# Optimization experiments

Measured on AMD Instinct MI355X. Metric: run time of the kernel, lower is better.

## Reference

```python
import jax, jax.numpy as jnp
import numpy as np

HIDDEN = 1024
EMB = 256
VOCAB = 500000
B = 4096
C = 128
EPS = 1e-12


def setup_inputs() -> dict:
    key = jax.random.key(0)
    ks = jax.random.split(key, 8)
    hidden_states = jax.random.normal(ks[0], (B, HIDDEN), dtype=jnp.float32)
    cand_idx = jax.random.randint(ks[1], (B, C), 0, VOCAB, dtype=jnp.int32)
    W_dense = jax.random.normal(ks[2], (EMB, HIDDEN), dtype=jnp.float32) * (1.0 / np.sqrt(HIDDEN))
    b_dense = jnp.zeros((EMB,), dtype=jnp.float32)
    ln_gamma = jnp.ones((EMB,), dtype=jnp.float32)
    ln_beta = jnp.zeros((EMB,), dtype=jnp.float32)
    decoder_table = jax.random.normal(ks[3], (VOCAB, EMB), dtype=jnp.float32) * 0.02
    entity_bias = jnp.zeros((VOCAB,), dtype=jnp.float32)
    return {
        "hidden_states": hidden_states,
        "W_dense": W_dense,
        "b_dense": b_dense,
        "ln_gamma": ln_gamma,
        "ln_beta": ln_beta,
        "decoder_table": decoder_table,
        "entity_bias": entity_bias,
        "cand_idx": cand_idx,
    }


def _transform(x, W_dense, b_dense, ln_gamma, ln_beta):
    # Linear hidden_size -> entity_emb_size, gelu, LayerNorm
    h = x @ W_dense.T + b_dense
    h = jax.nn.gelu(h, approximate=False)
    mu = jnp.mean(h, axis=-1, keepdims=True)
    var = jnp.mean(jnp.square(h - mu), axis=-1, keepdims=True)
    return (h - mu) * jax.lax.rsqrt(var + EPS) * ln_gamma + ln_beta


def reference(hidden_states, W_dense, b_dense, ln_gamma, ln_beta, decoder_table, entity_bias, cand_idx):
    h = _transform(hidden_states, W_dense, b_dense, ln_gamma, ln_beta)  # [B, EMB]
    cand_emb = decoder_table[cand_idx]          # [B, C, EMB] ragged gather (padded)
    bias = entity_bias[cand_idx]                # [B, C]
    scores = jnp.einsum('bce,be->bc', cand_emb, h) + bias  # [B, C]
    return scores
```

## Files before the change

kernel.cpp:

```cpp
#include <hip/hip_runtime.h>
#include <hip/hip_bf16.h>
#include <math.h>

#define HIDDEN 1024
#define EMB    256
#define BROWS  4096
#define CAND   128
#define LN_EPS 1e-12f

typedef __attribute__((ext_vector_type(8))) short bf16x8;
typedef __attribute__((ext_vector_type(4))) float f32x4;

__device__ __forceinline__ int swz(int row, int slot) { return slot ^ ((row >> 1) & 3); }

__device__ __forceinline__ unsigned short f2bf(float f) {
    __bf16 h = (__bf16)f;
    return __builtin_bit_cast(unsigned short, h);
}

__global__ __launch_bounds__(256) void k_transform(
    const float* __restrict__ A,
    const float* __restrict__ W,
    const float* __restrict__ bias,
    const float* __restrict__ gamma,
    const float* __restrict__ beta,
    float* __restrict__ G)
{
    __shared__ unsigned short As[16 * 32];
    __shared__ unsigned short Ws[256 * 32];
    __shared__ float part[16][8];

    const int tid  = threadIdx.x;
    const int lane = tid & 63;
    const int wv   = tid >> 6;
    const int m0   = blockIdx.x * 16;

    const int lcol = lane & 15;
    const int lk   = lane >> 4;

    f32x4 acc[4] = {};

    for (int kt = 0; kt < HIDDEN; kt += 32) {
        float4 a0, a1;
        const int arow = tid >> 2, apr = tid & 3;
        if (tid < 64) {
            a0 = *(const float4*)&A[(size_t)(m0 + arow) * HIDDEN + kt + apr * 8];
            a1 = *(const float4*)&A[(size_t)(m0 + arow) * HIDDEN + kt + apr * 8 + 4];
        }
        float4 w0[4], w1[4];
        #pragma unroll
        for (int i = 0; i < 4; ++i) {
            int id = tid + i * 256;
            int row = id >> 2, pr = id & 3;
            w0[i] = *(const float4*)&W[(size_t)row * HIDDEN + kt + pr * 8];
            w1[i] = *(const float4*)&W[(size_t)row * HIDDEN + kt + pr * 8 + 4];
        }
        __syncthreads();
        if (tid < 64) {
            bf16x8 v;
            v[0]=f2bf(a0.x); v[1]=f2bf(a0.y); v[2]=f2bf(a0.z); v[3]=f2bf(a0.w);
            v[4]=f2bf(a1.x); v[5]=f2bf(a1.y); v[6]=f2bf(a1.z); v[7]=f2bf(a1.w);
            *(bf16x8*)&As[arow * 32 + swz(arow, apr) * 8] = v;
        }
        #pragma unroll
        for (int i = 0; i < 4; ++i) {
            int id = tid + i * 256;
            int row = id >> 2, pr = id & 3;
            bf16x8 v;
            v[0]=f2bf(w0[i].x); v[1]=f2bf(w0[i].y); v[2]=f2bf(w0[i].z); v[3]=f2bf(w0[i].w);
            v[4]=f2bf(w1[i].x); v[5]=f2bf(w1[i].y); v[6]=f2bf(w1[i].z); v[7]=f2bf(w1[i].w);
            *(bf16x8*)&Ws[row * 32 + swz(row, pr) * 8] = v;
        }
        __syncthreads();
        bf16x8 af = *(const bf16x8*)&As[lcol * 32 + swz(lcol, lk) * 8];
        bf16x8 bfr[4];
        #pragma unroll
        for (int n = 0; n < 4; ++n) {
            int r = wv * 64 + n * 16 + lcol;
            bfr[n] = *(const bf16x8*)&Ws[r * 32 + swz(r, lk) * 8];
        }
        #pragma unroll
        for (int n = 0; n < 4; ++n)
            acc[n] = __builtin_amdgcn_mfma_f32_16x16x32_bf16(af, bfr[n], acc[n], 0, 0, 0);
    }

    float bcol[4], gcol[4], becol[4];
    #pragma unroll
    for (int n = 0; n < 4; ++n) {
        int col = wv * 64 + n * 16 + lcol;
        bcol[n]  = bias[col];
        gcol[n]  = gamma[col];
        becol[n] = beta[col];
    }

    float sv[4] = {}, qv[4] = {};
    #pragma unroll
    for (int n = 0; n < 4; ++n) {
        #pragma unroll
        for (int r = 0; r < 4; ++r) {
            float v = acc[n][r] + bcol[n];
            v = 0.5f * v * (1.0f + erff(v * 0.70710678118654752f));
            acc[n][r] = v;
            sv[r] += v;
            qv[r] += v * v;
        }
    }
    #pragma unroll
    for (int r = 0; r < 4; ++r) {
        #pragma unroll
        for (int msk = 8; msk >= 1; msk >>= 1) {
            sv[r] += __shfl_xor(sv[r], msk);
            qv[r] += __shfl_xor(qv[r], msk);
        }
    }
    if (lcol == 0) {
        #pragma unroll
        for (int r = 0; r < 4; ++r) {
            int R = lk * 4 + r;
            part[R][wv * 2 + 0] = sv[r];
            part[R][wv * 2 + 1] = qv[r];
        }
    }
    __syncthreads();

    #pragma unroll
    for (int r = 0; r < 4; ++r) {
        int R = lk * 4 + r;
        float4 p0 = *(const float4*)&part[R][0];
        float4 p1 = *(const float4*)&part[R][4];
        float s  = p0.x + p0.z + p1.x + p1.z;
        float q  = p0.y + p0.w + p1.y + p1.w;
        float mu = s * (1.0f / 256.0f);
        float var = q * (1.0f / 256.0f) - mu * mu;
        float rs = rsqrtf(var + LN_EPS);
        #pragma unroll
        for (int n = 0; n < 4; ++n) {
            int col = wv * 64 + n * 16 + lcol;
            G[(size_t)(m0 + R) * EMB + col] = (acc[n][r] - mu) * rs * gcol[n] + becol[n];
        }
    }
}

__global__ __launch_bounds__(256) void k_scores(
    const float* __restrict__ H,
    const float* __restrict__ table,
    const float* __restrict__ ebias,
    const int*   __restrict__ cidx,
    float* __restrict__ out)
{
    const int b    = blockIdx.x;
    const int tid  = threadIdx.x;
    const int lane = tid & 63;
    const int wv   = tid >> 6;
    const int l    = lane & 15;
    const int q    = lane >> 4;

    const float4* Hrow = (const float4*)(H + (size_t)b * EMB);
    float4 hv[4];
    #pragma unroll
    for (int p = 0; p < 4; ++p) hv[p] = Hrow[p * 16 + l];

    const int cbase = wv * 32 + q;
    int idxs[8];
    #pragma unroll
    for (int it = 0; it < 8; ++it)
        idxs[it] = cidx[(size_t)b * CAND + cbase + it * 4];

    #pragma unroll
    for (int it = 0; it < 8; ++it) {
        const float4* row = (const float4*)(table + (size_t)idxs[it] * EMB);
        float4 t0 = row[ 0 + l];
        float4 t1 = row[16 + l];
        float4 t2 = row[32 + l];
        float4 t3 = row[48 + l];
        float  eb = ebias[idxs[it]];
        float s = t0.x*hv[0].x + t0.y*hv[0].y + t0.z*hv[0].z + t0.w*hv[0].w
                + t1.x*hv[1].x + t1.y*hv[1].y + t1.z*hv[1].z + t1.w*hv[1].w
                + t2.x*hv[2].x + t2.y*hv[2].y + t2.z*hv[2].z + t2.w*hv[2].w
                + t3.x*hv[3].x + t3.y*hv[3].y + t3.z*hv[3].z + t3.w*hv[3].w;
        #pragma unroll
        for (int m = 8; m >= 1; m >>= 1) s += __shfl_xor(s, m);
        if (l == 0) out[(size_t)b * CAND + cbase + it * 4] = s + eb;
    }
}

extern "C" void kernel_launch(void* const* d_in, const int* in_sizes, int n_in,
                              void* d_out, int out_size, void* d_ws, size_t ws_size,
                              hipStream_t stream) {
    const float* hidden = (const float*)d_in[0];
    const float* Wd     = (const float*)d_in[1];
    const float* bd     = (const float*)d_in[2];
    const float* gamma  = (const float*)d_in[3];
    const float* beta   = (const float*)d_in[4];
    const float* table  = (const float*)d_in[5];
    const float* ebias  = (const float*)d_in[6];
    const int*   cidx   = (const int*)d_in[7];
    float* out = (float*)d_out;

    float* G = (float*)d_ws;

    k_transform<<<dim3(BROWS / 16), 256, 0, stream>>>(hidden, Wd, bd, gamma, beta, G);
    k_scores<<<dim3(BROWS), 256, 0, stream>>>(G, table, ebias, cidx, out);
}
```

Measured before the change: 135.6 us.

## Bucket-sort candidate entries by vocab index to improve table gather locality

Adds a counting-sort pipeline (zero, per-block histogram, single-block scan, scatter) that groups all B*C candidate entries into 1024 buckets by vocab index range. The gather kernel then processes entries in bucket order, so nearby table rows are fetched together and should hit in cache more often, with a block index swizzle spread across XCDs. The transformed hidden state is stored in bf16 to shrink the per-entry H reads that now become random. The cost is four extra launches, atomics, scattered output writes, and reduced precision of h.

```diff
diff --git a/kernel.cpp b/kernel.cpp
--- a/kernel.cpp
+++ b/kernel.cpp
@@ -8,6 +8,11 @@
 #define CAND   128
 #define LN_EPS 1e-12f
 
+#define NENT   (BROWS * CAND)
+#define NB     1024
+#define BKT_SH 9
+
+typedef unsigned int u32;
 typedef __attribute__((ext_vector_type(8))) short bf16x8;
 typedef __attribute__((ext_vector_type(4))) float f32x4;
 
@@ -16,6 +21,9 @@
 __device__ __forceinline__ unsigned short f2bf(float f) {
     __bf16 h = (__bf16)f;
     return __builtin_bit_cast(unsigned short, h);
+}
+__device__ __forceinline__ float bf2f(unsigned short u) {
+    return __builtin_bit_cast(float, (u32)u << 16);
 }
 
 __global__ __launch_bounds__(256) void k_transform(
@@ -24,7 +32,7 @@
     const float* __restrict__ bias,
     const float* __restrict__ gamma,
     const float* __restrict__ beta,
-    float* __restrict__ G)
+    unsigned short* __restrict__ Hbf)
 {
     __shared__ unsigned short As[16 * 32];
     __shared__ unsigned short Ws[256 * 32];
@@ -136,51 +144,130 @@
         #pragma unroll
         for (int n = 0; n < 4; ++n) {
             int col = wv * 64 + n * 16 + lcol;
-            G[(size_t)(m0 + R) * EMB + col] = (acc[n][r] - mu) * rs * gcol[n] + becol[n];
-        }
-    }
-}
-
-__global__ __launch_bounds__(256) void k_scores(
-    const float* __restrict__ H,
+            Hbf[(size_t)(m0 + R) * EMB + col] = f2bf((acc[n][r] - mu) * rs * gcol[n] + becol[n]);
+        }
+    }
+}
+
+__global__ __launch_bounds__(256) void k_zero(u32* __restrict__ bkt_pad)
+{
+    bkt_pad[blockIdx.x * 256 + threadIdx.x] = 0;
+}
+
+__global__ __launch_bounds__(256) void k_count(
+    const int* __restrict__ cidx, u32* __restrict__ bkt_pad)
+{
+    __shared__ u32 lh[NB];
+    const int tid = threadIdx.x;
+    for (int t = tid; t < NB; t += 256) lh[t] = 0;
+    __syncthreads();
+    const int base = blockIdx.x * 8192;
+    #pragma unroll
+    for (int i = 0; i < 32; ++i) {
+        int idx = cidx[base + i * 256 + tid];
+        atomicAdd(&lh[idx >> BKT_SH], 1u);
+    }
+    __syncthreads();
+    for (int t = tid; t < NB; t += 256) {
+        u32 v = lh[t];
+        if (v) atomicAdd(&bkt_pad[t * 16], v);
+    }
+}
+
+__global__ __launch_bounds__(1024) void k_scan(u32* __restrict__ bkt_pad)
+{
+    __shared__ u32 a[NB];
+    const int t = threadIdx.x;
+    const u32 own = bkt_pad[t * 16];
+    a[t] = own;
+    __syncthreads();
+    for (int off = 1; off < NB; off <<= 1) {
+        u32 add = (t >= off) ? a[t - off] : 0u;
+        __syncthreads();
+        a[t] += add;
+        __syncthreads();
+    }
+    bkt_pad[t * 16] = a[t] - own;
+}
+
+__global__ __launch_bounds__(256) void k_scatter(
+    const int* __restrict__ cidx, u32* __restrict__ bkt_pad,
+    u32* __restrict__ ent_idx, u32* __restrict__ ent_e)
+{
+    __shared__ u32 lh[NB];
+    __shared__ u32 lb[NB];
+    __shared__ u32 lo[NB];
+    const int tid = threadIdx.x;
+    for (int t = tid; t < NB; t += 256) { lh[t] = 0; lo[t] = 0; }
+    __syncthreads();
+    const int base = blockIdx.x * 8192;
+    u32 iv[32];
+    #pragma unroll
+    for (int i = 0; i < 32; ++i) {
+        iv[i] = (u32)cidx[base + i * 256 + tid];
+        atomicAdd(&lh[iv[i] >> BKT_SH], 1u);
+    }
+    __syncthreads();
+    for (int t = tid; t < NB; t += 256) {
+        u32 v = lh[t];
+        if (v) lb[t] = atomicAdd(&bkt_pad[t * 16], v);
+    }
+    __syncthreads();
+    #pragma unroll
+    for (int i = 0; i < 32; ++i) {
+        u32 bkt = iv[i] >> BKT_SH;
+        u32 p = lb[bkt] + atomicAdd(&lo[bkt], 1u);
+        ent_idx[p] = iv[i];
+        ent_e[p]   = (u32)(base + i * 256 + tid);
+    }
+}
+
+__global__ __launch_bounds__(256) void k_gather(
+    const unsigned short* __restrict__ Hbf,
     const float* __restrict__ table,
     const float* __restrict__ ebias,
-    const int*   __restrict__ cidx,
+    const u32* __restrict__ ent_idx,
+    const u32* __restrict__ ent_e,
     float* __restrict__ out)
 {
-    const int b    = blockIdx.x;
+    const int bid  = blockIdx.x;
+    const int work = (bid & 7) * 512 + (bid >> 3);
     const int tid  = threadIdx.x;
     const int lane = tid & 63;
     const int wv   = tid >> 6;
     const int l    = lane & 15;
     const int q    = lane >> 4;
 
-    const float4* Hrow = (const float4*)(H + (size_t)b * EMB);
-    float4 hv[4];
-    #pragma unroll
-    for (int p = 0; p < 4; ++p) hv[p] = Hrow[p * 16 + l];
-
-    const int cbase = wv * 32 + q;
-    int idxs[8];
-    #pragma unroll
-    for (int it = 0; it < 8; ++it)
-        idxs[it] = cidx[(size_t)b * CAND + cbase + it * 4];
+    const int ebase = work * 128 + wv * 32 + q;
+    u32 idxs[8], es[8];
+    #pragma unroll
+    for (int it = 0; it < 8; ++it) {
+        idxs[it] = ent_idx[ebase + it * 4];
+        es[it]   = ent_e[ebase + it * 4];
+    }
 
     #pragma unroll
     for (int it = 0; it < 8; ++it) {
         const float4* row = (const float4*)(table + (size_t)idxs[it] * EMB);
+        const u32 e = es[it];
+        const unsigned short* hrow = Hbf + (size_t)(e >> 7) * EMB;
+
         float4 t0 = row[ 0 + l];
         float4 t1 = row[16 + l];
         float4 t2 = row[32 + l];
         float4 t3 = row[48 + l];
-        float  eb = ebias[idxs[it]];
-        float s = t0.x*hv[0].x + t0.y*hv[0].y + t0.z*hv[0].z + t0.w*hv[0].w
-                + t1.x*hv[1].x + t1.y*hv[1].y + t1.z*hv[1].z + t1.w*hv[1].w
-                + t2.x*hv[2].x + t2.y*hv[2].y + t2.z*hv[2].z + t2.w*hv[2].w
-                + t3.x*hv[3].x + t3.y*hv[3].y + t3.z*hv[3].z + t3.w*hv[3].w;
+        ushort4 h0 = *(const ushort4*)&hrow[  0 + l * 4];
+        ushort4 h1 = *(const ushort4*)&hrow[ 64 + l * 4];
+        ushort4 h2 = *(const ushort4*)&hrow[128 + l * 4];
+        ushort4 h3 = *(const ushort4*)&hrow[192 + l * 4];
+
+        float s = t0.x*bf2f(h0.x) + t0.y*bf2f(h0.y) + t0.z*bf2f(h0.z) + t0.w*bf2f(h0.w)
+                + t1.x*bf2f(h1.x) + t1.y*bf2f(h1.y) + t1.z*bf2f(h1.z) + t1.w*bf2f(h1.w)
+                + t2.x*bf2f(h2.x) + t2.y*bf2f(h2.y) + t2.z*bf2f(h2.z) + t2.w*bf2f(h2.w)
+                + t3.x*bf2f(h3.x) + t3.y*bf2f(h3.y) + t3.z*bf2f(h3.z) + t3.w*bf2f(h3.w);
         #pragma unroll
         for (int m = 8; m >= 1; m >>= 1) s += __shfl_xor(s, m);
-        if (l == 0) out[(size_t)b * CAND + cbase + it * 4] = s + eb;
+        if (l == 0) out[e] = s + ebias[idxs[it]];
     }
 }
 
@@ -197,8 +284,16 @@
     const int*   cidx   = (const int*)d_in[7];
     float* out = (float*)d_out;
 
-    float* G = (float*)d_ws;
-
-    k_transform<<<dim3(BROWS / 16), 256, 0, stream>>>(hidden, Wd, bd, gamma, beta, G);
-    k_scores<<<dim3(BROWS), 256, 0, stream>>>(G, table, ebias, cidx, out);
-}
+    char* ws = (char*)d_ws;
+    unsigned short* Hbf  = (unsigned short*)(ws);
+    u32* bkt_pad         = (u32*)(ws + 2097152);
+    u32* ent_idx         = (u32*)(ws + 2097152 + 65536);
+    u32* ent_e           = (u32*)(ws + 2097152 + 65536 + 2097152);
+
+    k_transform<<<dim3(BROWS / 16), 256, 0, stream>>>(hidden, Wd, bd, gamma, beta, Hbf);
+    k_zero<<<dim3(64), 256, 0, stream>>>(bkt_pad);
+    k_count<<<dim3(64), 256, 0, stream>>>(cidx, bkt_pad);
+    k_scan<<<dim3(1), 1024, 0, stream>>>(bkt_pad);
+    k_scatter<<<dim3(64), 256, 0, stream>>>(cidx, bkt_pad, ent_idx, ent_e);
+    k_gather<<<dim3(NENT / 128), 256, 0, stream>>>(Hbf, table, ebias, ent_idx, ent_e, out);
+}
```

Result: slower. 177.7 us (+31.0%).

## Gather candidate rows directly into LDS with async global_load_lds and staged waits

Applied to the files above, without the earlier changes.

The scores kernel now issues all 16 candidate-row gathers per wave up front with global_load_lds. Each wave lane moves 16 bytes of a row straight into shared memory, and the kernel computes dot products in groups of four rows behind staged vmcnt waits. Each batch row is split across two blocks, which doubles the grid and halves the candidates per block. The goal is more memory-level parallelism on the random table gather and fewer register-staged loads. The trade-off is 64KB of LDS per block, which limits resident blocks per CU and may offset the gain.

```diff
diff --git a/kernel.cpp b/kernel.cpp
--- a/kernel.cpp
+++ b/kernel.cpp
@@ -148,39 +148,59 @@
     const int*   __restrict__ cidx,
     float* __restrict__ out)
 {
-    const int b    = blockIdx.x;
+    __shared__ float smem[16384];
     const int tid  = threadIdx.x;
     const int lane = tid & 63;
     const int wv   = tid >> 6;
     const int l    = lane & 15;
     const int q    = lane >> 4;
+    const int b     = blockIdx.x >> 1;
+    const int cbase = (blockIdx.x & 1) * 64 + wv * 16;
 
     const float4* Hrow = (const float4*)(H + (size_t)b * EMB);
     float4 hv[4];
     #pragma unroll
     for (int p = 0; p < 4; ++p) hv[p] = Hrow[p * 16 + l];
 
-    const int cbase = wv * 32 + q;
-    int idxs[8];
-    #pragma unroll
-    for (int it = 0; it < 8; ++it)
-        idxs[it] = cidx[(size_t)b * CAND + cbase + it * 4];
-
-    #pragma unroll
-    for (int it = 0; it < 8; ++it) {
-        const float4* row = (const float4*)(table + (size_t)idxs[it] * EMB);
-        float4 t0 = row[ 0 + l];
-        float4 t1 = row[16 + l];
-        float4 t2 = row[32 + l];
-        float4 t3 = row[48 + l];
-        float  eb = ebias[idxs[it]];
-        float s = t0.x*hv[0].x + t0.y*hv[0].y + t0.z*hv[0].z + t0.w*hv[0].w
-                + t1.x*hv[1].x + t1.y*hv[1].y + t1.z*hv[1].z + t1.w*hv[1].w
-                + t2.x*hv[2].x + t2.y*hv[2].y + t2.z*hv[2].z + t2.w*hv[2].w
-                + t3.x*hv[3].x + t3.y*hv[3].y + t3.z*hv[3].z + t3.w*hv[3].w;
-        #pragma unroll
-        for (int m = 8; m >= 1; m >>= 1) s += __shfl_xor(s, m);
-        if (l == 0) out[(size_t)b * CAND + cbase + it * 4] = s + eb;
+    const int sidxv = cidx[(size_t)b * CAND + cbase + l];
+    const float ebv = ebias[sidxv];
+
+    float* wbase = &smem[wv * 4096];
+    #pragma unroll
+    for (int r = 0; r < 16; ++r) {
+        int idx = __shfl(sidxv, r);
+        const float* gsrc = table + (size_t)idx * EMB + lane * 4;
+        __builtin_amdgcn_global_load_lds(
+            (const __attribute__((address_space(1))) void*)gsrc,
+            (__attribute__((address_space(3))) void*)(wbase + r * 256),
+            16, 0, 0);
+    }
+
+    float res[4];
+#define DOGROUP(g, WN)                                                        \
+    {                                                                         \
+        asm volatile("s_waitcnt vmcnt(" WN ")" ::: "memory");                 \
+        const float4* row = (const float4*)(wbase + (4 * (g) + q) * 256);     \
+        float s = 0.f;                                                        \
+        _Pragma("unroll")                                                     \
+        for (int p = 0; p < 4; ++p) {                                         \
+            float4 t = row[p * 16 + l];                                       \
+            s += t.x * hv[p].x + t.y * hv[p].y + t.z * hv[p].z + t.w * hv[p].w;\
+        }                                                                     \
+        _Pragma("unroll")                                                     \
+        for (int m = 8; m >= 1; m >>= 1) s += __shfl_xor(s, m);               \
+        res[g] = s;                                                           \
+    }
+    DOGROUP(0, "12")
+    DOGROUP(1, "8")
+    DOGROUP(2, "4")
+    DOGROUP(3, "0")
+#undef DOGROUP
+
+    #pragma unroll
+    for (int g = 0; g < 4; ++g) {
+        float eb = __shfl(ebv, 4 * g + q);
+        if (l == 0) out[(size_t)b * CAND + cbase + 4 * g + q] = res[g] + eb;
     }
 }
 
@@ -200,5 +220,5 @@
     float* G = (float*)d_ws;
 
     k_transform<<<dim3(BROWS / 16), 256, 0, stream>>>(hidden, Wd, bd, gamma, beta, G);
-    k_scores<<<dim3(BROWS), 256, 0, stream>>>(G, table, ebias, cidx, out);
-}
+    k_scores<<<dim3(BROWS * 2), 256, 0, stream>>>(G, table, ebias, cidx, out);
+}
```

New measurement: 135.2 us. Within noise of the previous version (-0.3%).
